# Kernel tuning notes

Measured on AMD Instinct MI355X. Metric: run time of the kernel, lower is better.

## Reference

```python
import jax, jax.numpy as jnp
import numpy as np
from jax import lax

# --- static config (Detectron defaults, C4-style RPN) ---
B, A_NUM, H, W = 8, 15, 100, 168
STRIDE = 8.0                 # 1.0 / spatial_scale
PRE_NMS = 2000               # RPN_PRE_NMS_TOP_N
POST_NMS = 1000              # RPN_POST_NMS_TOP_N
NMS_THRESH = 0.7
MIN_SIZE = 0.0
BBOX_XFORM_CLIP = float(np.log(1000.0 / 16.0))


def _make_anchors():
    sizes = np.array([32., 64., 128., 256., 512.])
    ratios = np.array([0.5, 1.0, 2.0])
    out = []
    for s in sizes:
        for r in ratios:
            w = s * np.sqrt(1.0 / r)
            h = s * np.sqrt(r)
            out.append([-(w - 1) / 2., -(h - 1) / 2., (w - 1) / 2., (h - 1) / 2.])
    return np.asarray(out, dtype=np.float32)  # [15, 4]


def setup_inputs() -> dict:
    key = jax.random.key(0)
    k1, k2 = jax.random.split(key)
    rpn_cls_prob = jax.random.uniform(k1, (B, A_NUM, H, W), jnp.float32)
    rpn_bbox_pred = jax.random.normal(k2, (B, 4 * A_NUM, H, W), jnp.float32) * 0.1
    im_info = jnp.tile(jnp.array([[H * STRIDE, W * STRIDE, 1.0]], jnp.float32), (B, 1))
    anchors = jnp.asarray(_make_anchors())
    return {"rpn_cls_prob": rpn_cls_prob, "rpn_bbox_pred": rpn_bbox_pred,
            "im_info": im_info, "anchors": anchors}


def _bbox_transform(anchors, deltas):
    # Detectron bbox_transform with weights (1,1,1,1)
    ws = anchors[:, 2] - anchors[:, 0] + 1.0
    hs = anchors[:, 3] - anchors[:, 1] + 1.0
    cx = anchors[:, 0] + 0.5 * ws
    cy = anchors[:, 1] + 0.5 * hs
    dx, dy = deltas[:, 0], deltas[:, 1]
    dw = jnp.minimum(deltas[:, 2], BBOX_XFORM_CLIP)
    dh = jnp.minimum(deltas[:, 3], BBOX_XFORM_CLIP)
    pcx = dx * ws + cx
    pcy = dy * hs + cy
    pw = jnp.exp(dw) * ws
    ph = jnp.exp(dh) * hs
    return jnp.stack([pcx - 0.5 * pw, pcy - 0.5 * ph,
                      pcx + 0.5 * pw - 1.0, pcy + 0.5 * ph - 1.0], axis=1)


def _nms_keep(boxes, valid, thresh):
    # Greedy NMS on score-sorted boxes, fixed-shape via lax.scan.
    P = boxes.shape[0]
    x1, y1, x2, y2 = boxes[:, 0], boxes[:, 1], boxes[:, 2], boxes[:, 3]
    areas = (x2 - x1 + 1.0) * (y2 - y1 + 1.0)
    iw = jnp.maximum(jnp.minimum(x2[:, None], x2[None, :]) - jnp.maximum(x1[:, None], x1[None, :]) + 1.0, 0.0)
    ih = jnp.maximum(jnp.minimum(y2[:, None], y2[None, :]) - jnp.maximum(y1[:, None], y1[None, :]) + 1.0, 0.0)
    inter = iw * ih
    iou = inter / (areas[:, None] + areas[None, :] - inter)  # [P, P]
    idxs = jnp.arange(P)

    def step(suppressed, inp):
        row, is_valid, i = inp
        keep_i = is_valid & (~suppressed[i])
        suppressed = suppressed | (keep_i & (row > thresh) & (idxs > i))
        return suppressed, keep_i

    _, keep = lax.scan(step, jnp.zeros((P,), bool), (iou, valid, idxs))
    return keep


def _one_image(scores, deltas, iminfo, all_anchors):
    # scores: [A,H,W], deltas: [4A,H,W] -> flat (h, w, a) ordering, matching
    # all_anchors built as (K, A) with K = h*W + w.
    scores_f = jnp.transpose(scores, (1, 2, 0)).reshape(-1)          # [K*A]
    deltas_f = jnp.transpose(deltas, (1, 2, 0)).reshape(-1, 4)       # [K*A, 4]
    top_s, top_i = lax.top_k(scores_f, PRE_NMS)
    props = _bbox_transform(all_anchors[top_i], deltas_f[top_i])
    # clip_tiled_boxes to image bounds
    wmax, hmax = iminfo[1] - 1.0, iminfo[0] - 1.0
    x1 = jnp.clip(props[:, 0], 0.0, wmax)
    y1 = jnp.clip(props[:, 1], 0.0, hmax)
    x2 = jnp.clip(props[:, 2], 0.0, wmax)
    y2 = jnp.clip(props[:, 3], 0.0, hmax)
    props = jnp.stack([x1, y1, x2, y2], axis=1)
    # _filter_boxes (mask instead of drop, for fixed shapes)
    ws = x2 - x1 + 1.0
    hs = y2 - y1 + 1.0
    ms = MIN_SIZE * iminfo[2]
    valid = (ws >= ms) & (hs >= ms) & ((x1 + ws / 2.0) < iminfo[1]) & ((y1 + hs / 2.0) < iminfo[0])
    keep = _nms_keep(props, valid, NMS_THRESH)
    # kept boxes first (stable sort preserves descending-score order), take POST_NMS
    order = jnp.argsort(jnp.where(keep, 0, 1).astype(jnp.int32))[:POST_NMS]
    kept = keep[order]
    boxes = jnp.where(kept[:, None], props[order], 0.0)
    probs = jnp.where(kept, top_s[order], 0.0)
    return boxes, probs


def reference(rpn_cls_prob, rpn_bbox_pred, im_info, anchors):
    shift_x = jnp.arange(W, dtype=jnp.float32) * STRIDE
    shift_y = jnp.arange(H, dtype=jnp.float32) * STRIDE
    sx, sy = jnp.meshgrid(shift_x, shift_y)                 # [H, W] each
    shifts = jnp.stack([sx.ravel(), sy.ravel(), sx.ravel(), sy.ravel()], axis=1)  # [K, 4]
    all_anchors = (anchors[None, :, :] + shifts[:, None, :]).reshape(-1, 4)       # [K*A, 4]
    boxes, probs = jax.vmap(_one_image, in_axes=(0, 0, 0, None))(
        rpn_cls_prob, rpn_bbox_pred, im_info, all_anchors)      # [B,P,4], [B,P]
    binds = jnp.broadcast_to(jnp.arange(B, dtype=jnp.float32)[:, None, None], (B, POST_NMS, 1))
    rois = jnp.concatenate([binds, boxes], axis=2).reshape(B * POST_NMS, 5)
    return rois, probs.reshape(-1)
```

## Files before the change

### kernel.cpp

```cpp
#include <hip/hip_runtime.h>
#include <hip/hip_bf16.h>
#include <math.h>

#define BN 8
#define AN 15
#define HH 100
#define WW 168
#define HW (HH*WW)
#define NPI (AN*HW)
#define NTOT (BN*NPI)
#define PRE 2000
#define POST 1000
#define CAP 4096
#define ROWW 32
#define NCHUNK 32
#define RSTRIDE 2048
#define EPB 4096
#define HBLK 62
#define GELEM 2048
#define GBLK 124

typedef unsigned int u32;
typedef unsigned long long u64;

#define OFF_H1     0
#define OFF_H2     507904
#define OFF_CSTAR  1015808
#define OFF_CCNT   1016832
#define OFF_THR    1017856
#define OFF_CAND   1018880
#define OFF_BOX    1281024
#define OFF_SCORE  1543168
#define OFF_VALID  1608704
#define OFF_MASK   1674240
#define OFF_DIAG   5868544

__device__ __forceinline__ u32 fmono(float s) {
  u32 u = __float_as_uint(s);
  return (u & 0x80000000u) ? ~u : (u | 0x80000000u);
}
__device__ __forceinline__ float funmono(u32 m) {
  u32 u = (m & 0x80000000u) ? (m ^ 0x80000000u) : ~m;
  return __uint_as_float(u);
}
__device__ __forceinline__ float areaf(float4 bx) {
  return __fmul_rn(__fadd_rn(__fsub_rn(bx.z, bx.x), 1.0f),
                   __fadd_rn(__fsub_rn(bx.w, bx.y), 1.0f));
}

#define BAR_LGKM() asm volatile("s_waitcnt lgkmcnt(0)\ns_barrier" ::: "memory")
#define WAVE_FENCE() asm volatile("" ::: "memory")

__global__ __launch_bounds__(256) void hist1_kernel(const float* __restrict__ cls,
                                                    u32* __restrict__ h1) {
  __shared__ u32 lh[2048];
  int b = blockIdx.y;
  int t = threadIdx.x;
  for (int q = t; q < 2048; q += 256) lh[q] = 0u;
  __syncthreads();
  int start = blockIdx.x * EPB;
  int end = min(start + EPB, NPI);
  const float* p = cls + (size_t)b * NPI;
  u32 copy = ((u32)t & 7u) << 8;
  for (int i = start + t; i < end; i += 256) {
    u32 m = fmono(p[i]);
    atomicAdd(&lh[copy | (m >> 24)], 1u);
  }
  __syncthreads();
  u32 s = 0;
#pragma unroll
  for (int cpy = 0; cpy < 8; ++cpy) s += lh[cpy * 256 + t];
  h1[((size_t)(b * HBLK) + blockIdx.x) * 256 + t] = s;
}

__global__ __launch_bounds__(256) void coarse_kernel(const u32* __restrict__ h1,
                                                     u32* __restrict__ cstar) {
  int b = blockIdx.x;
  int t = threadIdx.x;
  __shared__ u32 sfx[256];
  u32 s = 0;
  for (int blk = 0; blk < HBLK; ++blk) s += h1[((size_t)(b * HBLK) + blk) * 256 + t];
  sfx[t] = s;
  __syncthreads();
  for (int d = 1; d < 256; d <<= 1) {
    u32 add = (t + d < 256) ? sfx[t + d] : 0u;
    __syncthreads();
    sfx[t] += add;
    __syncthreads();
  }
  if (t == 0 && sfx[0] < (u32)PRE) { cstar[b * 32] = 0u; cstar[b * 32 + 1] = sfx[1]; }
  if (sfx[t] >= (u32)PRE && (t == 255 || sfx[t + 1] < (u32)PRE)) {
    cstar[b * 32] = (u32)t;
    cstar[b * 32 + 1] = (t == 255) ? 0u : sfx[t + 1];
  }
}

__global__ __launch_bounds__(256) void hist2_kernel(const float* __restrict__ cls,
                                                    const u32* __restrict__ cstar,
                                                    u32* __restrict__ h2) {
  __shared__ u32 lh[256];
  int b = blockIdx.y;
  int t = threadIdx.x;
  lh[t] = 0u;
  __syncthreads();
  u32 cs = cstar[b * 32];
  int start = blockIdx.x * EPB;
  int end = min(start + EPB, NPI);
  const float* p = cls + (size_t)b * NPI;
  for (int i = start + t; i < end; i += 256) {
    u32 m = fmono(p[i]);
    if ((m >> 24) == cs) atomicAdd(&lh[(m >> 16) & 0xFFu], 1u);
  }
  __syncthreads();
  h2[((size_t)(b * HBLK) + blockIdx.x) * 256 + t] = lh[t];
}

__global__ __launch_bounds__(256) void fine_kernel(const u32* __restrict__ h2,
                                                   const u32* __restrict__ cstar,
                                                   u32* __restrict__ thr,
                                                   u32* __restrict__ ccnt) {
  int b = blockIdx.x;
  int t = threadIdx.x;
  __shared__ u32 sfx[256];
  u32 s = 0;
  for (int blk = 0; blk < HBLK; ++blk) s += h2[((size_t)(b * HBLK) + blk) * 256 + t];
  sfx[t] = s;
  __syncthreads();
  for (int d = 1; d < 256; d <<= 1) {
    u32 add = (t + d < 256) ? sfx[t + d] : 0u;
    __syncthreads();
    sfx[t] += add;
    __syncthreads();
  }
  u32 cs = cstar[b * 32], base = cstar[b * 32 + 1];
  if (t == 0 && base + sfx[0] < (u32)PRE) thr[b * 32] = (cs << 8);
  if (base + sfx[t] >= (u32)PRE && (t == 255 || base + sfx[t + 1] < (u32)PRE))
    thr[b * 32] = (cs << 8) | (u32)t;
  if (t == 32) ccnt[b * 32] = 0u;
}

__global__ __launch_bounds__(256) void gather_kernel(
    const float* __restrict__ cls, const u32* __restrict__ thr,
    u32* __restrict__ ccnt, u64* __restrict__ cand) {
  int b = blockIdx.y;
  int t = threadIdx.x;
  int lane = t & 63, wid = t >> 6;
  int base_i = blockIdx.x * GELEM;
  const float* p = cls + (size_t)b * NPI;
  u32 T = thr[b * 32];
  __shared__ int wsum[4];
  __shared__ int wbase[4];
  __shared__ u32 baseSh;

  u32 mv[8];
  u32 flags = 0;
#pragma unroll
  for (int k = 0; k < 8; ++k) {
    int i = base_i + k * 256 + t;
    u32 m = 0;
    bool ok = false;
    if (i < NPI) { m = fmono(p[i]); ok = (m >> 16) >= T; }
    mv[k] = m;
    flags |= ok ? (1u << k) : 0u;
  }
  int ct = (int)__popc(flags);
  int inc = ct;
  for (int d = 1; d < 64; d <<= 1) {
    int n = __shfl_up(inc, d, 64);
    if (lane >= d) inc += n;
  }
  int excl = inc - ct;
  if (lane == 63) wsum[wid] = inc;
  __syncthreads();
  if (t == 0) {
    int acc = 0;
#pragma unroll
    for (int w = 0; w < 4; ++w) { wbase[w] = acc; acc += wsum[w]; }
    baseSh = acc ? atomicAdd(&ccnt[b * 32], (u32)acc) : 0u;
  }
  __syncthreads();
  if (!flags) return;
  u32 pos0 = baseSh + (u32)wbase[wid] + (u32)excl;
#pragma unroll
  for (int k = 0; k < 8; ++k) {
    if ((flags >> k) & 1u) {
      u32 pos = pos0 + (u32)__popc(flags & ((1u << k) - 1u));
      if (pos < CAP) {
        int i = base_i + k * 256 + t;
        int a = i / HW;
        int hw = i - a * HW;
        u32 ti = (u32)(hw * AN + a);
        cand[(size_t)b * CAP + pos] = ((u64)mv[k] << 32) | (u32)(~ti);
      }
    }
  }
}

__global__ __launch_bounds__(1024) void sort_transform_kernel(
    const u64* __restrict__ cand, const u32* __restrict__ ccnt,
    const u32* __restrict__ thr,
    const float* __restrict__ bbox, const float* __restrict__ iminfo,
    const float* __restrict__ anch,
    float4* __restrict__ boxes, float* __restrict__ scores, int* __restrict__ valid) {
  __shared__ u64 keys[CAP];
  __shared__ u64 keys2[2048];
  __shared__ u32 h24[256];
  __shared__ u32 sfx2[256];
  __shared__ u32 aboveSh, cmpCnt, t24Sh, cnt2Sh;
  int b = blockIdx.x;
  int t = threadIdx.x;
  int lane = t & 63;
  u32 cnt = ccnt[b * 32];
  if (cnt > CAP) cnt = CAP;
  u32 thr16v = thr[b * 32];
  for (int q = t; q < CAP; q += 1024) keys[q] = (q < (int)cnt) ? cand[(size_t)b * CAP + q] : 0ULL;
  if (t < 1024) { keys2[t] = 0ULL; keys2[t + 1024] = 0ULL; }
  if (t < 256) h24[t] = 0u;
  if (t == 0) { aboveSh = 0u; cmpCnt = 0u; }
  __syncthreads();

  for (int q0 = 0; q0 < CAP; q0 += 1024) {
    int q = q0 + t;
    u64 key = keys[q];
    u32 hi = (u32)(key >> 32);
    bool isReal = (q < (int)cnt);
    bool above = isReal && ((hi >> 16) > thr16v);
    u64 bal = __ballot(above);
    if (lane == 0 && bal) atomicAdd(&aboveSh, (u32)__popcll(bal));
    if (isReal && !above) atomicAdd(&h24[(hi >> 8) & 0xFFu], 1u);
  }
  __syncthreads();
  if (t < 256) sfx2[t] = h24[t];
  __syncthreads();
  for (int d = 1; d < 256; d <<= 1) {
    u32 add = (t < 256 && t + d < 256) ? sfx2[t + d] : 0u;
    __syncthreads();
    if (t < 256) sfx2[t] += add;
    __syncthreads();
  }
  if (t < 256) {
    u32 basev = aboveSh;
    if (t == 0 && basev + sfx2[0] < (u32)PRE) { t24Sh = 0u; cnt2Sh = basev + sfx2[0]; }
    if (basev + sfx2[t] >= (u32)PRE && (t == 255 || basev + sfx2[t + 1] < (u32)PRE)) {
      t24Sh = (u32)t; cnt2Sh = basev + sfx2[t];
    }
  }
  __syncthreads();
  u32 cnt2 = cnt2Sh;
  bool fallback = (cnt2 > 2048u);

  if (!fallback) {
    u32 t24 = (thr16v << 8) | t24Sh;
    for (int q0 = 0; q0 < CAP; q0 += 1024) {
      int q = q0 + t;
      u64 key = keys[q];
      u32 hi = (u32)(key >> 32);
      bool pass = (q < (int)cnt) && ((hi >> 8) >= t24);
      u64 bal = __ballot(pass);
      if (bal) {
        u32 wb = 0;
        if (lane == 0) wb = atomicAdd(&cmpCnt, (u32)__popcll(bal));
        wb = (u32)__shfl((int)wb, 0, 64);
        if (pass) {
          u32 rank = (u32)__popcll(bal & ((1ULL << lane) - 1ULL));
          keys2[wb + rank] = key;
        }
      }
    }
    __syncthreads();
    for (u32 k = 2; k <= 2048; k <<= 1) {
      for (u32 j = k >> 1; j > 0; j >>= 1) {
        if (j >= 128) __syncthreads();
        u32 idx = (u32)t;
        u32 base2 = ((idx & ~(j - 1)) << 1) | (idx & (j - 1));
        u32 partner = base2 + j;
        bool up2 = ((base2 & k) == 0);
        u64 A = keys2[base2], Bv = keys2[partner];
        bool sw = up2 ? (A < Bv) : (A > Bv);
        if (sw) { keys2[base2] = Bv; keys2[partner] = A; }
        if (j >= 128) __syncthreads();
        else WAVE_FENCE();
      }
    }
    __syncthreads();
  } else {
    for (u32 k = 2; k <= CAP; k <<= 1) {
      for (u32 j = k >> 1; j > 0; j >>= 1) {
        for (int p = 0; p < CAP / 2 / 1024; ++p) {
          u32 idx = (u32)t + (u32)p * 1024u;
          u32 base2 = ((idx & ~(j - 1)) << 1) | (idx & (j - 1));
          u32 partner = base2 + j;
          bool up2 = ((base2 & k) == 0);
          u64 A = keys[base2], Bv = keys[partner];
          bool sw = up2 ? (A < Bv) : (A > Bv);
          if (sw) { keys[base2] = Bv; keys[partner] = A; }
        }
        __syncthreads();
      }
    }
  }

  float im_h = iminfo[b * 3 + 0], im_w = iminfo[b * 3 + 1], im_s = iminfo[b * 3 + 2];
  float wmax = __fsub_rn(im_w, 1.0f), hmax = __fsub_rn(im_h, 1.0f);
  float msz = __fmul_rn(0.0f, im_s);
  const float BCLIP = (float)4.135166556742356;
  for (int q = t; q < PRE; q += 1024) {
    u64 key = fallback ? keys[q] : keys2[q];
    u32 i = ~((u32)key);
    if (q >= (int)cnt || i >= (u32)NPI) {
      boxes[b * RSTRIDE + q] = make_float4(0.f, 0.f, 0.f, 0.f);
      scores[b * RSTRIDE + q] = 0.f;
      valid[b * RSTRIDE + q] = 0;
      continue;
    }
    float sc = funmono((u32)(key >> 32));
    int a = (int)(i % AN);
    int pp = (int)(i / AN);
    int w = pp % WW;
    int h = pp / WW;
    float sx = (float)(w * 8), sy = (float)(h * 8);
    float ax1 = __fadd_rn(anch[a * 4 + 0], sx);
    float ay1 = __fadd_rn(anch[a * 4 + 1], sy);
    float ax2 = __fadd_rn(anch[a * 4 + 2], sx);
    float ay2 = __fadd_rn(anch[a * 4 + 3], sy);
    float wsA = __fadd_rn(__fsub_rn(ax2, ax1), 1.0f);
    float hsA = __fadd_rn(__fsub_rn(ay2, ay1), 1.0f);
    float cx = __fadd_rn(ax1, __fmul_rn(0.5f, wsA));
    float cy = __fadd_rn(ay1, __fmul_rn(0.5f, hsA));
    const float* dp = bbox + ((size_t)b * (4 * AN) + 4 * a) * HW + (size_t)h * WW + w;
    float dx = dp[0], dy = dp[HW], dwv = dp[2 * HW], dhv = dp[3 * HW];
    dwv = fminf(dwv, BCLIP);
    dhv = fminf(dhv, BCLIP);
    float pcx = __fadd_rn(__fmul_rn(dx, wsA), cx);
    float pcy = __fadd_rn(__fmul_rn(dy, hsA), cy);
    float pw = __fmul_rn((float)exp((double)dwv), wsA);
    float ph = __fmul_rn((float)exp((double)dhv), hsA);
    float hpw = __fmul_rn(0.5f, pw), hph = __fmul_rn(0.5f, ph);
    float x1 = __fsub_rn(pcx, hpw);
    float y1 = __fsub_rn(pcy, hph);
    float x2 = __fsub_rn(__fadd_rn(pcx, hpw), 1.0f);
    float y2 = __fsub_rn(__fadd_rn(pcy, hph), 1.0f);
    x1 = fminf(fmaxf(x1, 0.0f), wmax);
    y1 = fminf(fmaxf(y1, 0.0f), hmax);
    x2 = fminf(fmaxf(x2, 0.0f), wmax);
    y2 = fminf(fmaxf(y2, 0.0f), hmax);
    float ws2 = __fadd_rn(__fsub_rn(x2, x1), 1.0f);
    float hs2 = __fadd_rn(__fsub_rn(y2, y1), 1.0f);
    int v = (ws2 >= msz) && (hs2 >= msz) &&
            (__fadd_rn(x1, __fmul_rn(ws2, 0.5f)) < im_w) &&
            (__fadd_rn(y1, __fmul_rn(hs2, 0.5f)) < im_h);
    boxes[b * RSTRIDE + q] = make_float4(x1, y1, x2, y2);
    scores[b * RSTRIDE + q] = sc;
    valid[b * RSTRIDE + q] = v;
  }
}

__global__ __launch_bounds__(64) void nms_mask_kernel(const float4* __restrict__ boxes,
                                                      u64* __restrict__ mask,
                                                      u64* __restrict__ diag) {
  int jb = blockIdx.x, ib = blockIdx.y, b = blockIdx.z;
  if (jb < ib) return;
  int t = threadIdx.x;
  __shared__ float4 jbox[64];
  __shared__ float jarea[64];
  int jbase = jb * 64;
  int jcount = min(64, PRE - jbase);
  if (t < jcount) {
    float4 bj = boxes[b * RSTRIDE + jbase + t];
    jbox[t] = bj;
    jarea[t] = areaf(bj);
  }
  __syncthreads();
  int i = ib * 64 + t;
  if (i >= PRE) return;
  float4 bi = boxes[b * RSTRIDE + i];
  float ai = areaf(bi);
  u64 word = 0ULL;
  for (int jj = 0; jj < jcount; ++jj) {
    int j = jbase + jj;
    if (j <= i) continue;
    float4 bj = jbox[jj];
    float iw = fmaxf(__fadd_rn(__fsub_rn(fminf(bi.z, bj.z), fmaxf(bi.x, bj.x)), 1.0f), 0.0f);
    float ih = fmaxf(__fadd_rn(__fsub_rn(fminf(bi.w, bj.w), fmaxf(bi.y, bj.y)), 1.0f), 0.0f);
    float inter = __fmul_rn(iw, ih);
    float denom = __fsub_rn(__fadd_rn(ai, jarea[jj]), inter);
    float iou = inter / denom;
    if (iou > 0.7f) word |= (1ULL << jj);
  }
  mask[((size_t)(b * RSTRIDE) + i) * ROWW + jb] = word;
  if (jb == ib) diag[(size_t)b * RSTRIDE + i] = word;
}

__global__ __launch_bounds__(512) void seq_nms_kernel(
    const u64* __restrict__ mask, const u64* __restrict__ diag,
    const int* __restrict__ valid,
    const float4* __restrict__ boxes, const float* __restrict__ scores,
    float* __restrict__ out) {
  int b = blockIdx.x;
  int tid = threadIdx.x;
  int wid = tid >> 6, lane = tid & 63, lw = lane & 31, hf = lane >> 5;
  __shared__ u64 partial[16];
  __shared__ u64 keepbLDS;
  __shared__ u64 vbufLDS[NCHUNK];
  __shared__ u64 kbits_s[NCHUNK];
  __shared__ int chunkoff[NCHUNK];
  __shared__ int keeplist[PRE];
  __shared__ int Ksh;
  __shared__ int stopSh;

  if (tid < 16) partial[tid] = 0ULL;
  if (tid < NCHUNK) kbits_s[tid] = 0ULL;
  if (tid == 0) stopSh = 0;
  if (wid == 0) {
    for (int c = 0; c < NCHUNK; ++c) {
      int q = c * 64 + lane;
      int v = (q < PRE) ? valid[b * RSTRIDE + q] : 0;
      u64 bl = __ballot(v != 0);
      if (lane == 0) vbufLDS[c] = bl;
    }
  }
  __syncthreads();

  const u64* base = mask + (size_t)b * RSTRIDE * ROWW;
  const u64* dg = diag + (size_t)b * RSTRIDE;

  u64 rem = 0ULL;
  u64 Dv = 0ULL;
  if (wid == 0) Dv = dg[lane];
  int rb0 = wid * 8 + hf;
  int tot = 0;
  u64 cur0 = base[(size_t)(rb0 + 0) * ROWW + lw];
  u64 cur1 = base[(size_t)(rb0 + 2) * ROWW + lw];
  u64 cur2 = base[(size_t)(rb0 + 4) * ROWW + lw];
  u64 cur3 = base[(size_t)(rb0 + 6) * ROWW + lw];
  for (int c = 0; c < NCHUNK; ++c) {
    u64 n0 = 0, n1 = 0, n2 = 0, n3 = 0, Dnext = 0ULL;
    if (c + 1 < NCHUNK) {
      int c0n = (c + 1) * 64;
      n0 = base[(size_t)(c0n + rb0 + 0) * ROWW + lw];
      n1 = base[(size_t)(c0n + rb0 + 2) * ROWW + lw];
      n2 = base[(size_t)(c0n + rb0 + 4) * ROWW + lw];
      n3 = base[(size_t)(c0n + rb0 + 6) * ROWW + lw];
      if (wid == 0) Dnext = dg[(size_t)(c + 1) * 64 + lane];
    }
    if (wid == 0) {
      u64 nz = __ballot(Dv != 0ULL);
      u64 cv = partial[0];
#pragma unroll
      for (int s = 1; s < 16; ++s) cv |= partial[s];
      u32 clo = (u32)__builtin_amdgcn_readfirstlane((int)(u32)cv);
      u32 chi = (u32)__builtin_amdgcn_readfirstlane((int)(u32)(cv >> 32));
      u64 cl = ((u64)chi << 32) | clo;
      u64 vbv = vbufLDS[c];
      u32 vlo = (u32)__builtin_amdgcn_readfirstlane((int)(u32)vbv);
      u32 vhi = (u32)__builtin_amdgcn_readfirstlane((int)(u32)(vbv >> 32));
      u64 vb = ((u64)vhi << 32) | vlo;
      u32 dloA = (u32)Dv, dhiA = (u32)(Dv >> 32);
      u64 work = nz & vb;
      while (work) {
        int ii = __builtin_ctzll(work);
        work &= work - 1ULL;
        u32 dlo = (u32)__builtin_amdgcn_readlane((int)dloA, ii);
        u32 dhi = (u32)__builtin_amdgcn_readlane((int)dhiA, ii);
        u64 D = ((u64)dhi << 32) | dlo;
        u64 tt = ((~cl & vb) >> ii) & 1ULL;
        cl |= tt ? D : 0ULL;
      }
      u64 keepb = vb & ~cl;
      tot += (int)__popcll(keepb);
      if (lane == 0) {
        keepbLDS = keepb;
        kbits_s[c] = keepb;
        if (tot >= POST) stopSh = 1;
      }
    }
    BAR_LGKM();
    u64 keepb = keepbLDS;
    int stop = stopSh;
    rem |= cur0 & (0ULL - ((keepb >> (rb0 + 0)) & 1ULL));
    rem |= cur1 & (0ULL - ((keepb >> (rb0 + 2)) & 1ULL));
    rem |= cur2 & (0ULL - ((keepb >> (rb0 + 4)) & 1ULL));
    rem |= cur3 & (0ULL - ((keepb >> (rb0 + 6)) & 1ULL));
    int nw = (c + 1) & 31;
    if (lw == nw) partial[wid * 2 + hf] = rem;
    if (stop) break;
    BAR_LGKM();
    cur0 = n0; cur1 = n1; cur2 = n2; cur3 = n3;
    Dv = Dnext;
  }
  __syncthreads();

  if (wid == 0) {
    int pc = (lane < NCHUNK) ? (int)__popcll(kbits_s[lane]) : 0;
    int inc = pc;
    for (int d = 1; d < 64; d <<= 1) {
      int n = __shfl_up(inc, d, 64);
      if (lane >= d) inc += n;
    }
    if (lane < NCHUNK) chunkoff[lane] = inc - pc;
    if (lane == NCHUNK - 1) Ksh = inc;
  }
  __syncthreads();
  for (int c = wid * 4; c < wid * 4 + 4; ++c) {
    u64 word = kbits_s[c];
    if ((word >> lane) & 1ULL) {
      int rank = (int)__popcll(word & ((1ULL << lane) - 1ULL));
      keeplist[chunkoff[c] + rank] = c * 64 + lane;
    }
  }
  __syncthreads();
  int K = Ksh;

  float* rois = out;
  float* probs = out + (size_t)BN * POST * 5;
  for (int r = tid; r < POST; r += 512) {
    float x1 = 0.f, y1 = 0.f, x2 = 0.f, y2 = 0.f, pr = 0.f;
    if (r < K) {
      int i = keeplist[r];
      float4 bb = boxes[b * RSTRIDE + i];
      x1 = bb.x; y1 = bb.y; x2 = bb.z; y2 = bb.w;
      pr = scores[b * RSTRIDE + i];
    }
    size_t ro = (size_t)(b * POST + r) * 5;
    rois[ro + 0] = (float)b;
    rois[ro + 1] = x1; rois[ro + 2] = y1; rois[ro + 3] = x2; rois[ro + 4] = y2;
    probs[b * POST + r] = pr;
  }
}

extern "C" void kernel_launch(void* const* d_in, const int* in_sizes, int n_in,
                              void* d_out, int out_size, void* d_ws, size_t ws_size,
                              hipStream_t stream) {
  const float* cls    = (const float*)d_in[0];
  const float* bbox   = (const float*)d_in[1];
  const float* iminfo = (const float*)d_in[2];
  const float* anch   = (const float*)d_in[3];
  char* ws = (char*)d_ws;
  u32* h1    = (u32*)(ws + OFF_H1);
  u32* h2    = (u32*)(ws + OFF_H2);
  u32* cstar = (u32*)(ws + OFF_CSTAR);
  u32* ccnt  = (u32*)(ws + OFF_CCNT);
  u32* thr   = (u32*)(ws + OFF_THR);
  u64* cand  = (u64*)(ws + OFF_CAND);
  float4* boxes = (float4*)(ws + OFF_BOX);
  float* scores = (float*)(ws + OFF_SCORE);
  int* valid    = (int*)(ws + OFF_VALID);
  u64* mask     = (u64*)(ws + OFF_MASK);
  u64* diag     = (u64*)(ws + OFF_DIAG);
  float* out = (float*)d_out;

  hist1_kernel<<<dim3(HBLK, BN), 256, 0, stream>>>(cls, h1);
  coarse_kernel<<<BN, 256, 0, stream>>>(h1, cstar);
  hist2_kernel<<<dim3(HBLK, BN), 256, 0, stream>>>(cls, cstar, h2);
  fine_kernel<<<BN, 256, 0, stream>>>(h2, cstar, thr, ccnt);
  gather_kernel<<<dim3(GBLK, BN), 256, 0, stream>>>(cls, thr, ccnt, cand);
  sort_transform_kernel<<<BN, 1024, 0, stream>>>(cand, ccnt, thr, bbox, iminfo, anch,
                                                 boxes, scores, valid);
  nms_mask_kernel<<<dim3(32, 32, BN), 64, 0, stream>>>(boxes, mask, diag);
  seq_nms_kernel<<<BN, 512, 0, stream>>>(mask, diag, valid, boxes, scores, out);
}
```

Before: 194.7 us.

## Use wave-shuffle suffix scans, padded histogram copies, triangular NMS grid

Replaces the barrier-heavy 256-element shared-memory suffix scans in coarse, fine and sort kernels with a single-wave shuffle scan over 4 elements per lane. Histograms get more privatized copies with padded strides to cut LDS atomic contention and bank conflicts. The NMS mask launch becomes a compact triangular grid instead of launching and early-exiting lower-triangle blocks, and the bitonic sort drops redundant barriers. These trim latency in small serial kernels, but the barrier removal relies on the ordering between cross-wave and in-wave sort steps being correct.

```diff
diff --git a/kernel.cpp b/kernel.cpp
--- a/kernel.cpp
+++ b/kernel.cpp
@@ -51,25 +51,33 @@
 #define BAR_LGKM() asm volatile("s_waitcnt lgkmcnt(0)\ns_barrier" ::: "memory")
 #define WAVE_FENCE() asm volatile("" ::: "memory")
 
+__device__ __forceinline__ u32 wave_suffix_incl(u32 v, int lane) {
+  for (int d = 1; d < 64; d <<= 1) {
+    u32 n = (u32)__shfl_down((int)v, d, 64);
+    if (lane + d < 64) v += n;
+  }
+  return v;
+}
+
 __global__ __launch_bounds__(256) void hist1_kernel(const float* __restrict__ cls,
                                                     u32* __restrict__ h1) {
-  __shared__ u32 lh[2048];
+  __shared__ u32 lh[16 * 258];
   int b = blockIdx.y;
   int t = threadIdx.x;
-  for (int q = t; q < 2048; q += 256) lh[q] = 0u;
+  for (int q = t; q < 16 * 258; q += 256) lh[q] = 0u;
   __syncthreads();
   int start = blockIdx.x * EPB;
   int end = min(start + EPB, NPI);
   const float* p = cls + (size_t)b * NPI;
-  u32 copy = ((u32)t & 7u) << 8;
+  u32 copy = ((u32)t & 15u) * 258u;
   for (int i = start + t; i < end; i += 256) {
     u32 m = fmono(p[i]);
-    atomicAdd(&lh[copy | (m >> 24)], 1u);
+    atomicAdd(&lh[copy + (m >> 24)], 1u);
   }
   __syncthreads();
   u32 s = 0;
 #pragma unroll
-  for (int cpy = 0; cpy < 8; ++cpy) s += lh[cpy * 256 + t];
+  for (int cpy = 0; cpy < 16; ++cpy) s += lh[cpy * 258 + t];
   h1[((size_t)(b * HBLK) + blockIdx.x) * 256 + t] = s;
 }
 
@@ -77,42 +85,53 @@
                                                      u32* __restrict__ cstar) {
   int b = blockIdx.x;
   int t = threadIdx.x;
-  __shared__ u32 sfx[256];
+  __shared__ u32 cnts[256];
   u32 s = 0;
   for (int blk = 0; blk < HBLK; ++blk) s += h1[((size_t)(b * HBLK) + blk) * 256 + t];
-  sfx[t] = s;
-  __syncthreads();
-  for (int d = 1; d < 256; d <<= 1) {
-    u32 add = (t + d < 256) ? sfx[t + d] : 0u;
-    __syncthreads();
-    sfx[t] += add;
-    __syncthreads();
-  }
-  if (t == 0 && sfx[0] < (u32)PRE) { cstar[b * 32] = 0u; cstar[b * 32 + 1] = sfx[1]; }
-  if (sfx[t] >= (u32)PRE && (t == 255 || sfx[t + 1] < (u32)PRE)) {
-    cstar[b * 32] = (u32)t;
-    cstar[b * 32 + 1] = (t == 255) ? 0u : sfx[t + 1];
+  cnts[t] = s;
+  __syncthreads();
+  if (t < 64) {
+    int lane = t;
+    u32 v0 = cnts[4 * lane + 0], v1 = cnts[4 * lane + 1];
+    u32 v2 = cnts[4 * lane + 2], v3 = cnts[4 * lane + 3];
+    u32 ls3 = v3, ls2 = v2 + ls3, ls1 = v1 + ls2, ls0 = v0 + ls1;
+    u32 incl = wave_suffix_incl(ls0, lane);
+    u32 tail = incl - ls0;
+    u32 s0 = tail + ls0, s1 = tail + ls1, s2 = tail + ls2, s3 = tail + ls3;
+    u32 e0 = 4 * (u32)lane;
+    if (lane == 0 && s0 < (u32)PRE) { cstar[b * 32] = 0u; cstar[b * 32 + 1] = s1; }
+    if (s0 >= (u32)PRE && s1 < (u32)PRE) { cstar[b * 32] = e0 + 0; cstar[b * 32 + 1] = s1; }
+    if (s1 >= (u32)PRE && s2 < (u32)PRE) { cstar[b * 32] = e0 + 1; cstar[b * 32 + 1] = s2; }
+    if (s2 >= (u32)PRE && s3 < (u32)PRE) { cstar[b * 32] = e0 + 2; cstar[b * 32 + 1] = s3; }
+    if (s3 >= (u32)PRE && (e0 + 3 == 255u || tail < (u32)PRE)) {
+      cstar[b * 32] = e0 + 3;
+      cstar[b * 32 + 1] = (e0 + 3 == 255u) ? 0u : tail;
+    }
   }
 }
 
 __global__ __launch_bounds__(256) void hist2_kernel(const float* __restrict__ cls,
                                                     const u32* __restrict__ cstar,
                                                     u32* __restrict__ h2) {
-  __shared__ u32 lh[256];
+  __shared__ u32 lh[4 * 260];
   int b = blockIdx.y;
   int t = threadIdx.x;
-  lh[t] = 0u;
+  for (int q = t; q < 4 * 260; q += 256) lh[q] = 0u;
   __syncthreads();
   u32 cs = cstar[b * 32];
   int start = blockIdx.x * EPB;
   int end = min(start + EPB, NPI);
   const float* p = cls + (size_t)b * NPI;
+  u32 copy = ((u32)t & 3u) * 260u;
   for (int i = start + t; i < end; i += 256) {
     u32 m = fmono(p[i]);
-    if ((m >> 24) == cs) atomicAdd(&lh[(m >> 16) & 0xFFu], 1u);
-  }
-  __syncthreads();
-  h2[((size_t)(b * HBLK) + blockIdx.x) * 256 + t] = lh[t];
+    if ((m >> 24) == cs) atomicAdd(&lh[copy + ((m >> 16) & 0xFFu)], 1u);
+  }
+  __syncthreads();
+  u32 s = 0;
+#pragma unroll
+  for (int cpy = 0; cpy < 4; ++cpy) s += lh[cpy * 260 + t];
+  h2[((size_t)(b * HBLK) + blockIdx.x) * 256 + t] = s;
 }
 
 __global__ __launch_bounds__(256) void fine_kernel(const u32* __restrict__ h2,
@@ -121,22 +140,30 @@
                                                    u32* __restrict__ ccnt) {
   int b = blockIdx.x;
   int t = threadIdx.x;
-  __shared__ u32 sfx[256];
+  __shared__ u32 cnts[256];
   u32 s = 0;
   for (int blk = 0; blk < HBLK; ++blk) s += h2[((size_t)(b * HBLK) + blk) * 256 + t];
-  sfx[t] = s;
-  __syncthreads();
-  for (int d = 1; d < 256; d <<= 1) {
-    u32 add = (t + d < 256) ? sfx[t + d] : 0u;
-    __syncthreads();
-    sfx[t] += add;
-    __syncthreads();
-  }
-  u32 cs = cstar[b * 32], base = cstar[b * 32 + 1];
-  if (t == 0 && base + sfx[0] < (u32)PRE) thr[b * 32] = (cs << 8);
-  if (base + sfx[t] >= (u32)PRE && (t == 255 || base + sfx[t + 1] < (u32)PRE))
-    thr[b * 32] = (cs << 8) | (u32)t;
-  if (t == 32) ccnt[b * 32] = 0u;
+  cnts[t] = s;
+  __syncthreads();
+  if (t == 64) ccnt[b * 32] = 0u;
+  if (t < 64) {
+    int lane = t;
+    u32 cs = cstar[b * 32], base = cstar[b * 32 + 1];
+    u32 v0 = cnts[4 * lane + 0], v1 = cnts[4 * lane + 1];
+    u32 v2 = cnts[4 * lane + 2], v3 = cnts[4 * lane + 3];
+    u32 ls3 = v3, ls2 = v2 + ls3, ls1 = v1 + ls2, ls0 = v0 + ls1;
+    u32 incl = wave_suffix_incl(ls0, lane);
+    u32 tail = incl - ls0;
+    u32 s0 = base + tail + ls0, s1 = base + tail + ls1;
+    u32 s2 = base + tail + ls2, s3 = base + tail + ls3;
+    u32 sn = base + tail;
+    u32 e0 = 4 * (u32)lane;
+    if (lane == 0 && s0 < (u32)PRE) thr[b * 32] = (cs << 8);
+    if (s0 >= (u32)PRE && s1 < (u32)PRE) thr[b * 32] = (cs << 8) | (e0 + 0);
+    if (s1 >= (u32)PRE && s2 < (u32)PRE) thr[b * 32] = (cs << 8) | (e0 + 1);
+    if (s2 >= (u32)PRE && s3 < (u32)PRE) thr[b * 32] = (cs << 8) | (e0 + 2);
+    if (s3 >= (u32)PRE && (e0 + 3 == 255u || sn < (u32)PRE)) thr[b * 32] = (cs << 8) | (e0 + 3);
+  }
 }
 
 __global__ __launch_bounds__(256) void gather_kernel(
@@ -205,7 +232,6 @@
   __shared__ u64 keys[CAP];
   __shared__ u64 keys2[2048];
   __shared__ u32 h24[256];
-  __shared__ u32 sfx2[256];
   __shared__ u32 aboveSh, cmpCnt, t24Sh, cnt2Sh;
   int b = blockIdx.x;
   int t = threadIdx.x;
@@ -214,7 +240,7 @@
   if (cnt > CAP) cnt = CAP;
   u32 thr16v = thr[b * 32];
   for (int q = t; q < CAP; q += 1024) keys[q] = (q < (int)cnt) ? cand[(size_t)b * CAP + q] : 0ULL;
-  if (t < 1024) { keys2[t] = 0ULL; keys2[t + 1024] = 0ULL; }
+  keys2[t] = 0ULL; keys2[t + 1024] = 0ULL;
   if (t < 256) h24[t] = 0u;
   if (t == 0) { aboveSh = 0u; cmpCnt = 0u; }
   __syncthreads();
@@ -230,20 +256,22 @@
     if (isReal && !above) atomicAdd(&h24[(hi >> 8) & 0xFFu], 1u);
   }
   __syncthreads();
-  if (t < 256) sfx2[t] = h24[t];
-  __syncthreads();
-  for (int d = 1; d < 256; d <<= 1) {
-    u32 add = (t < 256 && t + d < 256) ? sfx2[t + d] : 0u;
-    __syncthreads();
-    if (t < 256) sfx2[t] += add;
-    __syncthreads();
-  }
-  if (t < 256) {
+  if (t < 64) {
     u32 basev = aboveSh;
-    if (t == 0 && basev + sfx2[0] < (u32)PRE) { t24Sh = 0u; cnt2Sh = basev + sfx2[0]; }
-    if (basev + sfx2[t] >= (u32)PRE && (t == 255 || basev + sfx2[t + 1] < (u32)PRE)) {
-      t24Sh = (u32)t; cnt2Sh = basev + sfx2[t];
-    }
+    u32 v0 = h24[4 * lane + 0], v1 = h24[4 * lane + 1];
+    u32 v2 = h24[4 * lane + 2], v3 = h24[4 * lane + 3];
+    u32 ls3 = v3, ls2 = v2 + ls3, ls1 = v1 + ls2, ls0 = v0 + ls1;
+    u32 incl = wave_suffix_incl(ls0, lane);
+    u32 tail = incl - ls0;
+    u32 s0 = basev + tail + ls0, s1 = basev + tail + ls1;
+    u32 s2 = basev + tail + ls2, s3 = basev + tail + ls3;
+    u32 sn = basev + tail;
+    u32 e0 = 4 * (u32)lane;
+    if (lane == 0 && s0 < (u32)PRE) { t24Sh = 0u; cnt2Sh = s0; }
+    if (s0 >= (u32)PRE && s1 < (u32)PRE) { t24Sh = e0 + 0; cnt2Sh = s0; }
+    if (s1 >= (u32)PRE && s2 < (u32)PRE) { t24Sh = e0 + 1; cnt2Sh = s1; }
+    if (s2 >= (u32)PRE && s3 < (u32)PRE) { t24Sh = e0 + 2; cnt2Sh = s2; }
+    if (s3 >= (u32)PRE && (e0 + 3 == 255u || sn < (u32)PRE)) { t24Sh = e0 + 3; cnt2Sh = s3; }
   }
   __syncthreads();
   u32 cnt2 = cnt2Sh;
@@ -270,7 +298,8 @@
     __syncthreads();
     for (u32 k = 2; k <= 2048; k <<= 1) {
       for (u32 j = k >> 1; j > 0; j >>= 1) {
-        if (j >= 128) __syncthreads();
+        bool cross = (j >= 128);
+        if (cross) __syncthreads();
         u32 idx = (u32)t;
         u32 base2 = ((idx & ~(j - 1)) << 1) | (idx & (j - 1));
         u32 partner = base2 + j;
@@ -278,7 +307,7 @@
         u64 A = keys2[base2], Bv = keys2[partner];
         bool sw = up2 ? (A < Bv) : (A > Bv);
         if (sw) { keys2[base2] = Bv; keys2[partner] = A; }
-        if (j >= 128) __syncthreads();
+        if (cross) { if (j == 128) __syncthreads(); }
         else WAVE_FENCE();
       }
     }
@@ -358,8 +387,10 @@
 __global__ __launch_bounds__(64) void nms_mask_kernel(const float4* __restrict__ boxes,
                                                       u64* __restrict__ mask,
                                                       u64* __restrict__ diag) {
-  int jb = blockIdx.x, ib = blockIdx.y, b = blockIdx.z;
-  if (jb < ib) return;
+  int L = blockIdx.x, b = blockIdx.y;
+  int ib = 0, rowlen = 32;
+  while (L >= rowlen) { L -= rowlen; rowlen--; ib++; }
+  int jb = ib + L;
   int t = threadIdx.x;
   __shared__ float4 jbox[64];
   __shared__ float jarea[64];
@@ -556,6 +587,6 @@
   gather_kernel<<<dim3(GBLK, BN), 256, 0, stream>>>(cls, thr, ccnt, cand);
   sort_transform_kernel<<<BN, 1024, 0, stream>>>(cand, ccnt, thr, bbox, iminfo, anch,
                                                  boxes, scores, valid);
-  nms_mask_kernel<<<dim3(32, 32, BN), 64, 0, stream>>>(boxes, mask, diag);
+  nms_mask_kernel<<<dim3(528, BN), 64, 0, stream>>>(boxes, mask, diag);
   seq_nms_kernel<<<BN, 512, 0, stream>>>(mask, diag, valid, boxes, scores, out);
 }
```

Measured after the change: 182.4 us. -6.4%, faster.
